# Performance work log

Hardware: AMD Instinct MI355X
Metric: run time of the kernel (lower is better)

The kernel has to match this reference:

```python
import jax, jax.numpy as jnp
import numpy as np
import math


def setup_inputs() -> dict:
    key = jax.random.key(0)
    kq, kk, kv = jax.random.split(key, 3)
    B, H, S, D = 8, 12, 4096, 64
    q = jax.random.normal(kq, (B, H, S, D), dtype=jnp.float32)
    k = jax.random.normal(kk, (B, H, S, D), dtype=jnp.float32)
    v = jax.random.normal(kv, (B, H, S, D), dtype=jnp.float32)
    return {"q": q, "k": k, "v": v}


def reference(q, k, v):
    B, H, S, D = q.shape
    topk = int(2 * math.sqrt(S))  # 128 for S=4096
    # importance = mean + std (torch.std is unbiased -> ddof=1)
    importance = q.mean(axis=-1) + jnp.std(q, axis=-1, ddof=1)  # [B,H,S]
    _, idx = jax.lax.top_k(importance, topk)  # [B,H,topk]
    idx_e = idx[..., None]  # [B,H,topk,1]
    q_s = jnp.take_along_axis(q, idx_e, axis=2)  # [B,H,topk,D]
    k_s = jnp.take_along_axis(k, idx_e, axis=2)
    v_s = jnp.take_along_axis(v, idx_e, axis=2)
    scores = jnp.einsum('bhtd,bhsd->bhts', q_s, k_s) / math.sqrt(D)
    attn = jax.nn.softmax(scores, axis=-1)
    out_s = jnp.einsum('bhts,bhsd->bhtd', attn, v_s)  # [B,H,topk,D]
    # scatter back into a full tensor (torch uses empty_like; we use zeros
    # for the unselected positions so the output is deterministic)
    bI = jnp.arange(B)[:, None, None]
    hI = jnp.arange(H)[None, :, None]
    out = jnp.zeros_like(v).at[bI, hI, idx].set(out_s)  # [B,H,S,D]
    Himg = int(math.sqrt(S))
    return out.reshape(B, -1, Himg, Himg)  # [B, H*D, Himg, Himg]
```

## Files before the change

kernel.cpp:

```cpp
#include <hip/hip_runtime.h>
#include <hip/hip_fp16.h>
#include <hip/hip_cooperative_groups.h>
#include <math.h>

#define BH_N 96
#define S_N 4096
#define D_N 64
#define TOPK 128
#define NBLK 384
#define UNITS_TOTAL 24576

typedef unsigned long long ull;
namespace cg = cooperative_groups;

__device__ __forceinline__ ull orderKey(double d) {
  ull u = (ull)__double_as_longlong(d);
  if (u & 0x8000000000000000ULL) u = ~u;
  else u |= 0x8000000000000000ULL;
  return u;
}

struct SharedMem {
  int red[2][4];
  int redG[4], redT[4], redS[4];
  int s_idx[TOPK];
  __align__(16) float sB[64 * 65];
  __align__(16) unsigned char uQP[32 * 132 * 2];
};

__device__ __forceinline__ void sel_attn_body(
    const float* __restrict__ q, const float* __restrict__ k,
    const float* __restrict__ v, const ull* __restrict__ keys,
    float* __restrict__ out, SharedMem& sm, int bh, int sub) {
  const int tid = threadIdx.x;
  const int lane = tid & 63;
  const int wv = tid >> 6;

  ull key[16];
  {
    const ull* kb = keys + (size_t)bh * S_N;
#pragma unroll
    for (int j = 0; j < 16; ++j) key[j] = kb[tid * 16 + j];
  }

  ull lo = 0ULL, hi = ~0ULL;
  int p = 0;
  while (lo < hi) {
    ull d = hi - lo;
    ull mid = lo + (d >> 1) + (d & 1ULL);
    int c = 0;
#pragma unroll
    for (int j = 0; j < 16; ++j) c += __popcll(__ballot(key[j] >= mid));
    if (lane == 0) sm.red[p][wv] = c;
    __syncthreads();
    int total = sm.red[p][0] + sm.red[p][1] + sm.red[p][2] + sm.red[p][3];
    if (total >= TOPK) lo = mid; else hi = mid - 1;
    p ^= 1;
  }
  const ull T = lo;

  {
    int cgt = 0, ctie = 0;
#pragma unroll
    for (int j = 0; j < 16; ++j) {
      cgt  += __popcll(__ballot(key[j] > T));
      ctie += __popcll(__ballot(key[j] == T));
    }
    if (lane == 0) { sm.redG[wv] = cgt; sm.redT[wv] = ctie; }
  }
  __syncthreads();
  const int need = TOPK - (sm.redG[0] + sm.redG[1] + sm.redG[2] + sm.redG[3]);
  int wTieBase = 0;
#pragma unroll
  for (int w = 0; w < 4; ++w) if (w < wv) wTieBase += sm.redT[w];

  const ull below = (1ULL << lane) - 1ULL;
  unsigned selBits = 0;
  {
    int lanesBelowTies = 0;
#pragma unroll
    for (int j = 0; j < 16; ++j)
      lanesBelowTies += __popcll(__ballot(key[j] == T) & below);
    int sameLane = 0;
#pragma unroll
    for (int j = 0; j < 16; ++j) {
      const bool isTie = (key[j] == T);
      const bool sel = (key[j] > T) ||
                       (isTie && (wTieBase + lanesBelowTies + sameLane) < need);
      if (sel) selBits |= (1u << j);
      sameLane += isTie ? 1 : 0;
    }
  }

  {
    int csel = 0, lanesBelowSel = 0;
#pragma unroll
    for (int j = 0; j < 16; ++j) {
      const ull ms = __ballot((selBits >> j) & 1u);
      csel += __popcll(ms);
      lanesBelowSel += __popcll(ms & below);
    }
    if (lane == 0) sm.redS[wv] = csel;
    __syncthreads();
    int pos = lanesBelowSel;
#pragma unroll
    for (int w = 0; w < 4; ++w) if (w < wv) pos += sm.redS[w];
#pragma unroll
    for (int j = 0; j < 16; ++j) {
      if ((selBits >> j) & 1u) { sm.s_idx[pos] = tid * 16 + j; ++pos; }
    }
  }
  __syncthreads();

  float* sQ = reinterpret_cast<float*>(sm.uQP);
  __half* sP = reinterpret_cast<__half*>(sm.uQP);
  float* sB = sm.sB;

  const size_t base = (size_t)bh * S_N * D_N;
  const int rgrp = tid >> 4;
  const int c4 = (tid & 15) * 4;
  const int rr = tid >> 4;
  const int cc = tid & 15;

#pragma unroll
  for (int it = 0; it < 2; ++it) {
    int r = it * 16 + rgrp;
    int srow = sm.s_idx[sub * 32 + r];
    float4 val = *reinterpret_cast<const float4*>(q + base + (size_t)srow * D_N + c4);
    sQ[r * 65 + c4 + 0] = val.x; sQ[r * 65 + c4 + 1] = val.y;
    sQ[r * 65 + c4 + 2] = val.z; sQ[r * 65 + c4 + 3] = val.w;
  }

  float acc[2][8];
#pragma unroll
  for (int j = 0; j < 2; ++j)
#pragma unroll
    for (int m = 0; m < 8; ++m) acc[j][m] = 0.f;

  for (int h = 0; h < 2; ++h) {
    __syncthreads();
#pragma unroll
    for (int it = 0; it < 4; ++it) {
      int r = it * 16 + rgrp;
      int srow = sm.s_idx[h * 64 + r];
      float4 val = *reinterpret_cast<const float4*>(k + base + (size_t)srow * D_N + c4);
      sB[r * 65 + c4 + 0] = val.x; sB[r * 65 + c4 + 1] = val.y;
      sB[r * 65 + c4 + 2] = val.z; sB[r * 65 + c4 + 3] = val.w;
    }
    __syncthreads();
    for (int kk = 0; kk < 64; kk += 2) {
#pragma unroll
      for (int u = 0; u < 2; ++u) {
        float qv0 = sQ[(2 * rr + 0) * 65 + kk + u];
        float qv1 = sQ[(2 * rr + 1) * 65 + kk + u];
        float kv[4];
#pragma unroll
        for (int m = 0; m < 4; ++m) kv[m] = sB[(cc * 4 + m) * 65 + kk + u];
#pragma unroll
        for (int m = 0; m < 4; ++m) {
          acc[0][h * 4 + m] += qv0 * kv[m];
          acc[1][h * 4 + m] += qv1 * kv[m];
        }
      }
    }
  }

  float rmax[2], rsum[2];
#pragma unroll
  for (int j = 0; j < 2; ++j) {
    float mx = acc[j][0];
#pragma unroll
    for (int m = 1; m < 8; ++m) mx = fmaxf(mx, acc[j][m]);
    rmax[j] = mx;
  }
#pragma unroll
  for (int mm = 1; mm < 16; mm <<= 1)
#pragma unroll
    for (int j = 0; j < 2; ++j) rmax[j] = fmaxf(rmax[j], __shfl_xor(rmax[j], mm, 64));
#pragma unroll
  for (int j = 0; j < 2; ++j) {
    float sum = 0.f;
#pragma unroll
    for (int m = 0; m < 8; ++m) {
      float pe = __expf(0.125f * (acc[j][m] - rmax[j]));
      acc[j][m] = pe;
      sum += pe;
    }
    rsum[j] = sum;
  }
#pragma unroll
  for (int mm = 1; mm < 16; mm <<= 1)
#pragma unroll
    for (int j = 0; j < 2; ++j) rsum[j] += __shfl_xor(rsum[j], mm, 64);

  __syncthreads();

#pragma unroll
  for (int j = 0; j < 2; ++j) {
    float rinv = 1.f / rsum[j];
#pragma unroll
    for (int h2 = 0; h2 < 2; ++h2)
#pragma unroll
      for (int m = 0; m < 4; ++m) {
        int col = h2 * 64 + cc * 4 + m;
        sP[(2 * rr + j) * 132 + col] = __float2half_rn(acc[j][h2 * 4 + m] * rinv);
      }
  }

  float acc2[2][4];
#pragma unroll
  for (int j = 0; j < 2; ++j)
#pragma unroll
    for (int m = 0; m < 4; ++m) acc2[j][m] = 0.f;

  for (int h = 0; h < 2; ++h) {
    __syncthreads();
#pragma unroll
    for (int it = 0; it < 4; ++it) {
      int r = it * 16 + rgrp;
      int srow = sm.s_idx[h * 64 + r];
      float4 val = *reinterpret_cast<const float4*>(v + base + (size_t)srow * D_N + c4);
      sB[r * 65 + c4 + 0] = val.x; sB[r * 65 + c4 + 1] = val.y;
      sB[r * 65 + c4 + 2] = val.z; sB[r * 65 + c4 + 3] = val.w;
    }
    __syncthreads();
    for (int s2 = 0; s2 < 64; ++s2) {
      int scol = h * 64 + s2;
      float pj0 = __half2float(sP[(2 * rr + 0) * 132 + scol]);
      float pj1 = __half2float(sP[(2 * rr + 1) * 132 + scol]);
      float vm[4];
#pragma unroll
      for (int m = 0; m < 4; ++m) vm[m] = sB[s2 * 65 + cc * 4 + m];
#pragma unroll
      for (int m = 0; m < 4; ++m) {
        acc2[0][m] += pj0 * vm[m];
        acc2[1][m] += pj1 * vm[m];
      }
    }
  }

#pragma unroll
  for (int j = 0; j < 2; ++j) {
    int srow = sm.s_idx[sub * 32 + 2 * rr + j];
    float4 val;
    val.x = acc2[j][0]; val.y = acc2[j][1]; val.z = acc2[j][2]; val.w = acc2[j][3];
    *reinterpret_cast<float4*>(out + base + (size_t)srow * D_N + cc * 4) = val;
  }
}

__global__ __launch_bounds__(256, 2)
void fused_coop(const float* __restrict__ q, const float* __restrict__ k,
                const float* __restrict__ v, float* __restrict__ out,
                ull* __restrict__ keys) {
  __shared__ SharedMem sm;
  {
    const int bid = blockIdx.x;
    const int tid = threadIdx.x;
    float4 z; z.x = z.y = z.z = z.w = 0.f;
#pragma unroll 1
    for (int u0 = 0; u0 < UNITS_TOTAL / NBLK; u0 += 8) {
      size_t offs[8];
      float4 val[8];
#pragma unroll
      for (int i = 0; i < 8; ++i) {
        const size_t unit = (size_t)bid * (UNITS_TOTAL / NBLK) + (u0 + i);
        offs[i] = unit * 1024 + (size_t)tid * 4;
        val[i] = *reinterpret_cast<const float4*>(q + offs[i]);
      }
#pragma unroll
      for (int i = 0; i < 8; ++i)
        *reinterpret_cast<float4*>(out + offs[i]) = z;
#pragma unroll
      for (int i = 0; i < 8; ++i) {
        double s  = (double)val[i].x + (double)val[i].y + (double)val[i].z + (double)val[i].w;
        double ss = (double)val[i].x * val[i].x + (double)val[i].y * val[i].y +
                    (double)val[i].z * val[i].z + (double)val[i].w * val[i].w;
#pragma unroll
        for (int m = 1; m < 16; m <<= 1) {
          s  += __shfl_xor(s, m, 64);
          ss += __shfl_xor(ss, m, 64);
        }
        if ((tid & 15) == 0) {
          double mean = s * (1.0 / 64.0);
          double var = (ss - s * s * (1.0 / 64.0)) * (1.0 / 63.0);
          if (var < 0.0) var = 0.0;
          const size_t unit = (size_t)bid * (UNITS_TOTAL / NBLK) + (u0 + i);
          keys[unit * 16 + (tid >> 4)] = orderKey(mean + sqrt(var));
        }
      }
    }
  }

  cg::this_grid().sync();

  sel_attn_body(q, k, v, keys, out, sm, blockIdx.x >> 2, blockIdx.x & 3);
}

__global__ __launch_bounds__(256)
void imp_zero_kernel(const float* __restrict__ q, float* __restrict__ out,
                     ull* __restrict__ keys) {
  const int tid = threadIdx.x;
  const size_t off = (size_t)blockIdx.x * 1024 + (size_t)tid * 4;
  const float4 v = *reinterpret_cast<const float4*>(q + off);
  float4 z; z.x = z.y = z.z = z.w = 0.f;
  *reinterpret_cast<float4*>(out + off) = z;

  double s  = (double)v.x + (double)v.y + (double)v.z + (double)v.w;
  double ss = (double)v.x * v.x + (double)v.y * v.y +
              (double)v.z * v.z + (double)v.w * v.w;
#pragma unroll
  for (int m = 1; m < 16; m <<= 1) {
    s  += __shfl_xor(s, m, 64);
    ss += __shfl_xor(ss, m, 64);
  }
  if ((tid & 15) == 0) {
    double mean = s * (1.0 / 64.0);
    double var = (ss - s * s * (1.0 / 64.0)) * (1.0 / 63.0);
    if (var < 0.0) var = 0.0;
    keys[(size_t)blockIdx.x * 16 + (tid >> 4)] = orderKey(mean + sqrt(var));
  }
}

__global__ __launch_bounds__(256, 2)
void sel_attn_kernel(const float* __restrict__ q, const float* __restrict__ k,
                     const float* __restrict__ v, const ull* __restrict__ keys,
                     float* __restrict__ out) {
  __shared__ SharedMem sm;
  sel_attn_body(q, k, v, keys, out, sm, blockIdx.x >> 2, blockIdx.x & 3);
}

extern "C" void kernel_launch(void* const* d_in, const int* in_sizes, int n_in,
                              void* d_out, int out_size, void* d_ws, size_t ws_size,
                              hipStream_t stream) {
  const float* q = (const float*)d_in[0];
  const float* k = (const float*)d_in[1];
  const float* v = (const float*)d_in[2];
  float* out = (float*)d_out;
  ull* keys = (ull*)d_ws;

  static int coop_ok = -1;
  if (coop_ok != 0) {
    void* args[] = {(void*)&q, (void*)&k, (void*)&v, (void*)&out, (void*)&keys};
    hipError_t e = hipLaunchCooperativeKernel((void*)fused_coop, dim3(NBLK),
                                              dim3(256), args, 0, stream);
    if (e == hipSuccess) { coop_ok = 1; return; }
    coop_ok = 0;
    (void)hipGetLastError();
  }

  imp_zero_kernel<<<UNITS_TOTAL, 256, 0, stream>>>(q, out, keys);
  sel_attn_kernel<<<NBLK, 256, 0, stream>>>(q, k, v, keys, out);
}
```

Before: 293.4 us.

## Replace cooperative grid sync with per-head completion counters in one launch

Drops the cooperative launch and its grid-wide barrier. A single kernel now runs 24576 producer blocks that compute importance keys and zero the output, then bump a per-(batch,head) atomic counter. It also runs 384 consumer blocks that spin on their head's counter before running the selection-attention body. This lets attention for a head start as soon as that head's keys are ready, instead of waiting for the whole grid. It adds a memset launch and relies on producer blocks being scheduled ahead of the spinning consumers, which risks a deadlock or stalls if consumers occupy slots early.

```diff
diff --git a/kernel.cpp b/kernel.cpp
--- a/kernel.cpp
+++ b/kernel.cpp
@@ -1,17 +1,15 @@
 #include <hip/hip_runtime.h>
 #include <hip/hip_fp16.h>
-#include <hip/hip_cooperative_groups.h>
 #include <math.h>
 
 #define BH_N 96
 #define S_N 4096
 #define D_N 64
 #define TOPK 128
-#define NBLK 384
+#define NCONS 384
 #define UNITS_TOTAL 24576
 
 typedef unsigned long long ull;
-namespace cg = cooperative_groups;
 
 __device__ __forceinline__ ull orderKey(double d) {
   ull u = (ull)__double_as_longlong(d);
@@ -248,85 +246,56 @@
   }
 }
 
-__global__ __launch_bounds__(256, 2)
-void fused_coop(const float* __restrict__ q, const float* __restrict__ k,
+__global__ __launch_bounds__(256)
+void fused_flag(const float* __restrict__ q, const float* __restrict__ k,
                 const float* __restrict__ v, float* __restrict__ out,
-                ull* __restrict__ keys) {
+                ull* __restrict__ keys, int* __restrict__ done) {
   __shared__ SharedMem sm;
-  {
-    const int bid = blockIdx.x;
-    const int tid = threadIdx.x;
+  const int bid = blockIdx.x;
+  const int tid = threadIdx.x;
+
+  if (bid < UNITS_TOTAL) {
+    const size_t off = (size_t)bid * 1024 + (size_t)tid * 4;
+    const float4 val = *reinterpret_cast<const float4*>(q + off);
     float4 z; z.x = z.y = z.z = z.w = 0.f;
-#pragma unroll 1
-    for (int u0 = 0; u0 < UNITS_TOTAL / NBLK; u0 += 8) {
-      size_t offs[8];
-      float4 val[8];
-#pragma unroll
-      for (int i = 0; i < 8; ++i) {
-        const size_t unit = (size_t)bid * (UNITS_TOTAL / NBLK) + (u0 + i);
-        offs[i] = unit * 1024 + (size_t)tid * 4;
-        val[i] = *reinterpret_cast<const float4*>(q + offs[i]);
-      }
-#pragma unroll
-      for (int i = 0; i < 8; ++i)
-        *reinterpret_cast<float4*>(out + offs[i]) = z;
-#pragma unroll
-      for (int i = 0; i < 8; ++i) {
-        double s  = (double)val[i].x + (double)val[i].y + (double)val[i].z + (double)val[i].w;
-        double ss = (double)val[i].x * val[i].x + (double)val[i].y * val[i].y +
-                    (double)val[i].z * val[i].z + (double)val[i].w * val[i].w;
-#pragma unroll
-        for (int m = 1; m < 16; m <<= 1) {
-          s  += __shfl_xor(s, m, 64);
-          ss += __shfl_xor(ss, m, 64);
-        }
-        if ((tid & 15) == 0) {
-          double mean = s * (1.0 / 64.0);
-          double var = (ss - s * s * (1.0 / 64.0)) * (1.0 / 63.0);
-          if (var < 0.0) var = 0.0;
-          const size_t unit = (size_t)bid * (UNITS_TOTAL / NBLK) + (u0 + i);
-          keys[unit * 16 + (tid >> 4)] = orderKey(mean + sqrt(var));
-        }
-      }
-    }
-  }
-
-  cg::this_grid().sync();
-
-  sel_attn_body(q, k, v, keys, out, sm, blockIdx.x >> 2, blockIdx.x & 3);
-}
-
-__global__ __launch_bounds__(256)
-void imp_zero_kernel(const float* __restrict__ q, float* __restrict__ out,
-                     ull* __restrict__ keys) {
-  const int tid = threadIdx.x;
-  const size_t off = (size_t)blockIdx.x * 1024 + (size_t)tid * 4;
-  const float4 v = *reinterpret_cast<const float4*>(q + off);
-  float4 z; z.x = z.y = z.z = z.w = 0.f;
-  *reinterpret_cast<float4*>(out + off) = z;
-
-  double s  = (double)v.x + (double)v.y + (double)v.z + (double)v.w;
-  double ss = (double)v.x * v.x + (double)v.y * v.y +
-              (double)v.z * v.z + (double)v.w * v.w;
-#pragma unroll
-  for (int m = 1; m < 16; m <<= 1) {
-    s  += __shfl_xor(s, m, 64);
-    ss += __shfl_xor(ss, m, 64);
-  }
-  if ((tid & 15) == 0) {
-    double mean = s * (1.0 / 64.0);
-    double var = (ss - s * s * (1.0 / 64.0)) * (1.0 / 63.0);
-    if (var < 0.0) var = 0.0;
-    keys[(size_t)blockIdx.x * 16 + (tid >> 4)] = orderKey(mean + sqrt(var));
-  }
-}
-
-__global__ __launch_bounds__(256, 2)
-void sel_attn_kernel(const float* __restrict__ q, const float* __restrict__ k,
-                     const float* __restrict__ v, const ull* __restrict__ keys,
-                     float* __restrict__ out) {
-  __shared__ SharedMem sm;
-  sel_attn_body(q, k, v, keys, out, sm, blockIdx.x >> 2, blockIdx.x & 3);
+    *reinterpret_cast<float4*>(out + off) = z;
+
+    double s  = (double)val.x + (double)val.y + (double)val.z + (double)val.w;
+    double ss = (double)val.x * val.x + (double)val.y * val.y +
+                (double)val.z * val.z + (double)val.w * val.w;
+#pragma unroll
+    for (int m = 1; m < 16; m <<= 1) {
+      s  += __shfl_xor(s, m, 64);
+      ss += __shfl_xor(ss, m, 64);
+    }
+    if ((tid & 15) == 0) {
+      double mean = s * (1.0 / 64.0);
+      double var = (ss - s * s * (1.0 / 64.0)) * (1.0 / 63.0);
+      if (var < 0.0) var = 0.0;
+      keys[(size_t)bid * 16 + (tid >> 4)] = orderKey(mean + sqrt(var));
+    }
+
+    __syncthreads();
+    if (tid == 0) {
+      __hip_atomic_fetch_add(&done[bid >> 8], 1, __ATOMIC_RELEASE,
+                             __HIP_MEMORY_SCOPE_AGENT);
+    }
+    return;
+  }
+
+  const int cid = bid - UNITS_TOTAL;
+  const int bh = cid >> 2;
+  const int sub = cid & 3;
+
+  if (tid == 0) {
+    while (__hip_atomic_load(&done[bh], __ATOMIC_RELAXED,
+                             __HIP_MEMORY_SCOPE_AGENT) < 256)
+      __builtin_amdgcn_s_sleep(4);
+  }
+  __syncthreads();
+  __threadfence();
+
+  sel_attn_body(q, k, v, keys, out, sm, bh, sub);
 }
 
 extern "C" void kernel_launch(void* const* d_in, const int* in_sizes, int n_in,
@@ -337,17 +306,8 @@
   const float* v = (const float*)d_in[2];
   float* out = (float*)d_out;
   ull* keys = (ull*)d_ws;
-
-  static int coop_ok = -1;
-  if (coop_ok != 0) {
-    void* args[] = {(void*)&q, (void*)&k, (void*)&v, (void*)&out, (void*)&keys};
-    hipError_t e = hipLaunchCooperativeKernel((void*)fused_coop, dim3(NBLK),
-                                              dim3(256), args, 0, stream);
-    if (e == hipSuccess) { coop_ok = 1; return; }
-    coop_ok = 0;
-    (void)hipGetLastError();
-  }
-
-  imp_zero_kernel<<<UNITS_TOTAL, 256, 0, stream>>>(q, out, keys);
-  sel_attn_kernel<<<NBLK, 256, 0, stream>>>(q, k, v, keys, out);
+  int* done = (int*)((char*)d_ws + (size_t)BH_N * S_N * 8);
+
+  hipMemsetAsync(done, 0, BH_N * sizeof(int), stream);
+  fused_flag<<<UNITS_TOTAL + NCONS, 256, 0, stream>>>(q, k, v, out, keys, done);
 }
```

Result: slower. 1.107 ms (+277.1%).
